# Optimization experiments

Measured on AMD Instinct MI355X. Metric: run time of the kernel, lower is better.

The kernel has to match this reference:

```python
import jax, jax.numpy as jnp
import numpy as np

N = 100_000      # num nodes
E = 1_600_000    # num edges
IN = 128         # in_channels
H = 256          # hidden_channels
BN_EPS = 1e-5
L2_EPS = 1e-12


def setup_inputs() -> dict:
    key = jax.random.key(0)
    ks = jax.random.split(key, 12)
    x = jax.random.normal(ks[0], (N, IN), dtype=jnp.float32)
    edge_index = jax.random.randint(ks[1], (2, E), 0, N, dtype=jnp.int64)
    edge_weight = jax.random.uniform(ks[2], (E,), dtype=jnp.float32)
    s_in = 1.0 / np.sqrt(IN)
    s_h = 1.0 / np.sqrt(H)
    return {
        "x": x,
        "edge_index": edge_index,
        "edge_weight": edge_weight,
        # lin0 (skip projection)
        "W0": jax.random.normal(ks[3], (H, IN), jnp.float32) * s_in,
        "b0": jnp.zeros((H,), jnp.float32),
        # conv1
        "W1": jax.random.normal(ks[4], (H, IN), jnp.float32) * s_in,
        "b1": jnp.zeros((H,), jnp.float32),
        "g1": jnp.ones((H,), jnp.float32),
        "be1": jnp.zeros((H,), jnp.float32),
        "m1": jax.random.normal(ks[5], (H,), jnp.float32) * 0.1,
        "v1": jax.random.uniform(ks[6], (H,), jnp.float32, 0.5, 1.5),
        # conv2
        "W2": jax.random.normal(ks[7], (H, H), jnp.float32) * s_h,
        "b2": jnp.zeros((H,), jnp.float32),
        "g2": jnp.ones((H,), jnp.float32),
        "be2": jnp.zeros((H,), jnp.float32),
        "m2": jax.random.normal(ks[8], (H,), jnp.float32) * 0.1,
        "v2": jax.random.uniform(ks[9], (H,), jnp.float32, 0.5, 1.5),
        # classifier
        "Wc": jax.random.normal(ks[10], (2, H), jnp.float32) * s_h,
        "bc": jnp.zeros((2,), jnp.float32),
    }


def _gcn_conv(x, src, dst, ew, W, b):
    """PyG GCNConv: D^-1/2 (A + I) D^-1/2 X W^T + b (self-loop weight 1)."""
    h = x @ W.T                                            # [N, out]
    deg = jax.ops.segment_sum(ew, dst, num_segments=N) + 1.0  # weighted in-degree incl. self-loop
    dinv = jnp.where(deg > 0, jax.lax.rsqrt(deg), 0.0)     # [N]
    norm = dinv[src] * ew * dinv[dst]                      # [E]
    agg = jax.ops.segment_sum(norm[:, None] * h[src], dst, num_segments=N)
    agg = agg + (dinv * dinv)[:, None] * h                 # self-loop term
    return agg + b


def _bn_eval(x, g, beta, m, v):
    return (x - m) * jax.lax.rsqrt(v + BN_EPS) * g + beta


def _l2norm(x):
    n = jnp.sqrt(jnp.sum(x * x, axis=1, keepdims=True))
    return x / jnp.maximum(n, L2_EPS)


def reference(x, edge_index, edge_weight, W0, b0, W1, b1, g1, be1, m1, v1,
              W2, b2, g2, be2, m2, v2, Wc, bc):
    src, dst = edge_index[0], edge_index[1]
    x0 = x @ W0.T + b0                                     # lin0 skip
    x1 = _gcn_conv(x, src, dst, edge_weight, W1, b1)
    x1 = jax.nn.relu(_bn_eval(x1, g1, be1, m1, v1))        # dropout = identity (eval)
    x1 = _l2norm(x1) + 0.2 * x0
    x2 = _gcn_conv(x1, src, dst, edge_weight, W2, b2)
    x2 = _bn_eval(x2, g2, be2, m2, v2)
    x2 = _l2norm(x2)
    embeddings = x2 + 0.5 * x1
    logits = embeddings @ Wc.T + bc
    return embeddings, logits
```

## Files before the change

kernel.cpp:

```cpp
#include <hip/hip_runtime.h>

#define NN 100000
#define EE 1600000
#define NBIN 391
#define CAPB 4864
#define TSCL 63.5f
#define TINV (1.0f / 63.5f)
#define XS   21.166666f
#define XSI  (6.0f / 127.0f)
#define WQS  16384.0f
#define WQI  (1.0f / 16384.0f)

typedef short bf16x8 __attribute__((ext_vector_type(8)));
typedef float f32x4 __attribute__((ext_vector_type(4)));

__device__ __forceinline__ float bl(unsigned int u) { return __uint_as_float(u << 16); }
__device__ __forceinline__ float bh(unsigned int u) { return __uint_as_float(u & 0xffff0000u); }
__device__ __forceinline__ unsigned short f2b(float f) {
  unsigned int u = __float_as_uint(f);
  return (unsigned short)((u + 0x7fffu + ((u >> 16) & 1u)) >> 16);
}
__device__ __forceinline__ float wsum(float v) {
#pragma unroll
  for (int o = 32; o; o >>= 1) v += __shfl_xor(v, o);
  return v;
}
__device__ __forceinline__ void g2l16(const void* g, void* l) {
  __builtin_amdgcn_global_load_lds((const __attribute__((address_space(1))) unsigned int*)g,
                                   (__attribute__((address_space(3))) unsigned int*)l, 16, 0, 0);
}
__device__ __forceinline__ int q8(float v, float lim, float sc) {
  return __float2int_rn(fminf(fmaxf(v, -lim), lim) * sc) & 0xff;
}
__device__ __forceinline__ int sx8(int u, int sh) { return (int)(signed char)(u >> sh); }

__global__ void k_zero(int* cnt, int n) {
  int i = blockIdx.x * 256 + threadIdx.x;
  if (i < n) cnt[i] = 0;
}

__global__ __launch_bounds__(256) void k_build(
    const int* __restrict__ src, const int* __restrict__ dst,
    const float* __restrict__ ew, int* gcnt, uint2* __restrict__ gbuf,
    const float* __restrict__ x, unsigned short* __restrict__ xb,
    unsigned int* __restrict__ xq8,
    const float* __restrict__ W1, const float* __restrict__ W0,
    const float* __restrict__ W2, unsigned short* __restrict__ Wcat,
    unsigned short* __restrict__ W2b)
{
  const int b = blockIdx.x;
  if (b < 391) {
    __shared__ uint2 est[4096];
    __shared__ int lhist[NBIN], lbase[NBIN], lcur[NBIN];
    const int tid = threadIdx.x;
    for (int t = tid; t < NBIN; t += 256) { lhist[t] = 0; lcur[t] = 0; }
    __syncthreads();
    const int e0 = b * 4096;
    const int ne = min(4096, EE - e0);
    for (int k = tid; k < ne; k += 256) {
      int e = e0 + k;
      int d = dst[e];
      int bin = d >> 8, low = d & 255;
      int q = min(__float2int_rn(ew[e] * 32768.0f), 32767);
      est[k] = make_uint2((unsigned)src[e],
                          ((unsigned)bin << 23) | ((unsigned)q << 8) | (unsigned)low);
      atomicAdd(&lhist[bin], 1);
    }
    __syncthreads();
    for (int t = tid; t < NBIN; t += 256)
      lbase[t] = lhist[t] ? atomicAdd(&gcnt[t], lhist[t]) : 0;
    __syncthreads();
    for (int k = tid; k < ne; k += 256) {
      uint2 E = est[k];
      int bin = E.y >> 23;
      int p = lbase[bin] + atomicAdd(&lcur[bin], 1);
      if (p < CAPB) gbuf[(size_t)bin * CAPB + p] = make_uint2(E.x, E.y & 0x7FFFFFu);
    }
  } else if (b < 12891) {
    int i = (b - 391) * 256 + threadIdx.x;
    float4 v = ((const float4*)x)[i];
    uint2 o;
    o.x = (unsigned int)f2b(v.x) | ((unsigned int)f2b(v.y) << 16);
    o.y = (unsigned int)f2b(v.z) | ((unsigned int)f2b(v.w) << 16);
    ((uint2*)xb)[i] = o;
    unsigned int p8 = (unsigned)q8(v.x, 6.f, XS) | ((unsigned)q8(v.y, 6.f, XS) << 8) |
                      ((unsigned)q8(v.z, 6.f, XS) << 16) | ((unsigned)q8(v.w, 6.f, XS) << 24);
    xq8[i] = p8;
  } else {
    int wb = b - 12891;
    const float* in;
    unsigned short* out;
    int idx;
    if (wb < 32)      { in = W1; out = Wcat;             idx = wb * 256 + threadIdx.x; }
    else if (wb < 64) { in = W0; out = Wcat + 256 * 128; idx = (wb - 32) * 256 + threadIdx.x; }
    else              { in = W2; out = W2b;              idx = (wb - 64) * 256 + threadIdx.x; }
    float4 v = ((const float4*)in)[idx];
    uint2 o;
    o.x = (unsigned int)f2b(v.x) | ((unsigned int)f2b(v.y) << 16);
    o.y = (unsigned int)f2b(v.z) | ((unsigned int)f2b(v.w) << 16);
    ((uint2*)out)[idx] = o;
  }
}

__global__ __launch_bounds__(256) void k_phase2(
    const uint2* __restrict__ gbuf, const int* __restrict__ gcnt,
    unsigned int* __restrict__ csr, int2* __restrict__ ntab, float* __restrict__ dinv)
{
  __shared__ uint2 ebuf[CAPB];
  __shared__ unsigned int obuf[CAPB];
  __shared__ int hist[256];
  __shared__ float wsm[256];
  __shared__ int cur[256];
  __shared__ int psum[256];
  const int g = blockIdx.x, tid = threadIdx.x;
  hist[tid] = 0; wsm[tid] = 0.f;
  __syncthreads();
  const int cn = min(gcnt[g], CAPB);
  for (int j = tid; j < cn; j += 256) {
    uint2 E = gbuf[(size_t)g * CAPB + j];
    ebuf[j] = E;
    int low = E.y & 255;
    atomicAdd(&hist[low], 1);
    atomicAdd(&wsm[low], (float)(E.y >> 8) * (1.0f / 32768.0f));
  }
  __syncthreads();
  int v = hist[tid];
  psum[tid] = v;
  __syncthreads();
  for (int off = 1; off < 256; off <<= 1) {
    int t = (tid >= off) ? psum[tid - off] : 0;
    __syncthreads();
    psum[tid] += t;
    __syncthreads();
  }
  int ex = psum[tid] - v;
  cur[tid] = ex;
  int node = g * 256 + tid;
  if (node < NN) {
    ntab[node] = make_int2(g * CAPB + ex, v);
    dinv[node] = rsqrtf(wsm[tid] + 1.0f);
  }
  __syncthreads();
  for (int j = tid; j < cn; j += 256) {
    uint2 E = ebuf[j];
    int low = E.y & 255;
    int p = atomicAdd(&cur[low], 1);
    obuf[p] = E.x | ((E.y >> 8) << 17);
  }
  __syncthreads();
  for (int j = tid; j < cn; j += 256) csr[(size_t)g * CAPB + j] = obuf[j];
}

__global__ __launch_bounds__(256) void k_aggregate8(
    const signed char* __restrict__ xq8, const int2* __restrict__ ntab,
    const unsigned int* __restrict__ csr, const float* __restrict__ dinv,
    unsigned short* __restrict__ ax)
{
  __shared__ int2 sm[4][64];
  const int wid = threadIdx.x >> 6, lane = threadIdx.x & 63;
  const int i = blockIdx.x * 4 + wid;
  const int2 nt = ntab[i];
  const int beg = nt.x, cn = nt.y;
  int acc0 = 0, acc1 = 0;
  for (int base = 0; base < cn; base += 64) {
    const int chunk = min(64, cn - base);
    int2 ent;
    if (lane < chunk) {
      unsigned int u = csr[beg + base + lane];
      int s = (int)(u & 0x1FFFFu);
      float nr = (float)(u >> 17) * (1.0f / 32768.0f) * dinv[s];
      ent = make_int2(s, __float2int_rn(nr * WQS));
    } else {
      ent = make_int2(i, 0);
    }
    sm[wid][lane] = ent;
    for (int sub = 0; sub < chunk; sub += 8) {
      int2 e[8];
#pragma unroll
      for (int k = 0; k < 8; ++k) e[k] = sm[wid][sub + k];
      int u[8];
#pragma unroll
      for (int k = 0; k < 8; ++k)
        u[k] = (int)*(const unsigned short*)(xq8 + (size_t)e[k].x * 128 + lane * 2);
#pragma unroll
      for (int k = 0; k < 8; ++k) {
        acc0 += __mul24(e[k].y, sx8(u[k], 0));
        acc1 += __mul24(e[k].y, sx8(u[k], 8));
      }
    }
  }
  const float di = dinv[i];
  const int di_q = __float2int_rn(di * WQS);
  int us = (int)*(const unsigned short*)(xq8 + (size_t)i * 128 + lane * 2);
  acc0 += __mul24(di_q, sx8(us, 0));
  acc1 += __mul24(di_q, sx8(us, 8));
  const float f = di * XSI * WQI;
  float r0 = f * (float)acc0;
  float r1 = f * (float)acc1;
  unsigned int o = (unsigned int)f2b(r0) | ((unsigned int)f2b(r1) << 16);
  *(unsigned int*)(ax + (size_t)i * 128 + lane * 2) = o;
}

__global__ __launch_bounds__(256) void k_mgemm(
    const unsigned short* __restrict__ A0, const unsigned short* __restrict__ A1, int nsplit,
    const unsigned short* __restrict__ B, unsigned short* __restrict__ C,
    int M, int K, int ldc)
{
  __shared__ __align__(16) unsigned short Als[128 * 64];
  __shared__ __align__(16) unsigned short Bls[128 * 64];
  const int tid = threadIdx.x;
  const int w = tid >> 6, l = tid & 63;
  const int m0 = blockIdx.x * 128, n0 = blockIdx.y * 128;
  const unsigned short* __restrict__ A = (n0 < nsplit) ? A0 : A1;
  const int wr = w >> 1, wc = w & 1;
  const int lr = l >> 3;
  const int lc = l & 7;
  const int fr = l & 15;
  const int fk = l >> 4;
  f32x4 acc[4][4];
#pragma unroll
  for (int m = 0; m < 4; ++m)
#pragma unroll
    for (int n = 0; n < 4; ++n)
#pragma unroll
      for (int q = 0; q < 4; ++q) acc[m][n][q] = 0.f;

  for (int k0 = 0; k0 < K; k0 += 64) {
#pragma unroll
    for (int i2 = 0; i2 < 4; ++i2) {
      const int ob = (w * 4 + i2) * 1024;
      const int r = (ob >> 7) + lr;
      const int c = lc ^ (r & 7);
      int rg = m0 + r; if (rg >= M) rg = M - 1;
      g2l16(A + (size_t)rg * K + k0 + c * 8, (char*)Als + ob);
      g2l16(B + (size_t)(n0 + r) * K + k0 + c * 8, (char*)Bls + ob);
    }
    __syncthreads();
#pragma unroll
    for (int ks = 0; ks < 2; ++ks) {
      bf16x8 af[4], bfr[4];
#pragma unroll
      for (int m = 0; m < 4; ++m) {
        const int r = wr * 64 + m * 16 + fr;
        const int cc = (ks * 4 + fk) ^ (r & 7);
        af[m] = *(const bf16x8*)((const char*)Als + r * 128 + cc * 16);
      }
#pragma unroll
      for (int n = 0; n < 4; ++n) {
        const int r = wc * 64 + n * 16 + fr;
        const int cc = (ks * 4 + fk) ^ (r & 7);
        bfr[n] = *(const bf16x8*)((const char*)Bls + r * 128 + cc * 16);
      }
#pragma unroll
      for (int m = 0; m < 4; ++m)
#pragma unroll
        for (int n = 0; n < 4; ++n)
          acc[m][n] = __builtin_amdgcn_mfma_f32_16x16x32_bf16(af[m], bfr[n], acc[m][n], 0, 0, 0);
    }
    __syncthreads();
  }
#pragma unroll
  for (int m = 0; m < 4; ++m) {
    const int rbase = m0 + wr * 64 + m * 16 + fk * 4;
#pragma unroll
    for (int n = 0; n < 4; ++n) {
      const int col = n0 + wc * 64 + n * 16 + fr;
#pragma unroll
      for (int q = 0; q < 4; ++q) {
        const int row = rbase + q;
        if (row < M) C[(size_t)row * ldc + col] = f2b(acc[m][n][q]);
      }
    }
  }
}

__global__ __launch_bounds__(256) void k_mgemmq(
    const unsigned short* __restrict__ A, const unsigned short* __restrict__ B,
    signed char* __restrict__ t8)
{
  __shared__ __align__(16) unsigned short Als[128 * 64];
  __shared__ __align__(16) unsigned short Bls[128 * 64];
  const int tid = threadIdx.x;
  const int w = tid >> 6, l = tid & 63;
  const int m0 = blockIdx.x * 128, n0 = blockIdx.y * 128;
  const int wr = w >> 1, wc = w & 1;
  const int lr = l >> 3;
  const int lc = l & 7;
  const int fr = l & 15;
  const int fk = l >> 4;
  f32x4 acc[4][4];
#pragma unroll
  for (int m = 0; m < 4; ++m)
#pragma unroll
    for (int n = 0; n < 4; ++n)
#pragma unroll
      for (int q = 0; q < 4; ++q) acc[m][n][q] = 0.f;

  for (int k0 = 0; k0 < 256; k0 += 64) {
#pragma unroll
    for (int i2 = 0; i2 < 4; ++i2) {
      const int ob = (w * 4 + i2) * 1024;
      const int r = (ob >> 7) + lr;
      const int c = lc ^ (r & 7);
      int rg = m0 + r; if (rg >= NN) rg = NN - 1;
      g2l16(A + (size_t)rg * 256 + k0 + c * 8, (char*)Als + ob);
      g2l16(B + (size_t)(n0 + r) * 256 + k0 + c * 8, (char*)Bls + ob);
    }
    __syncthreads();
#pragma unroll
    for (int ks = 0; ks < 2; ++ks) {
      bf16x8 af[4], bfr[4];
#pragma unroll
      for (int m = 0; m < 4; ++m) {
        const int r = wr * 64 + m * 16 + fr;
        const int cc = (ks * 4 + fk) ^ (r & 7);
        af[m] = *(const bf16x8*)((const char*)Als + r * 128 + cc * 16);
      }
#pragma unroll
      for (int n = 0; n < 4; ++n) {
        const int r = wc * 64 + n * 16 + fr;
        const int cc = (ks * 4 + fk) ^ (r & 7);
        bfr[n] = *(const bf16x8*)((const char*)Bls + r * 128 + cc * 16);
      }
#pragma unroll
      for (int m = 0; m < 4; ++m)
#pragma unroll
        for (int n = 0; n < 4; ++n)
          acc[m][n] = __builtin_amdgcn_mfma_f32_16x16x32_bf16(af[m], bfr[n], acc[m][n], 0, 0, 0);
    }
    __syncthreads();
  }
#pragma unroll
  for (int m = 0; m < 4; ++m) {
    const int rbase = m0 + wr * 64 + m * 16 + fk * 4;
#pragma unroll
    for (int n = 0; n < 4; ++n) {
      const int col = n0 + wc * 64 + n * 16 + fr;
#pragma unroll
      for (int q = 0; q < 4; ++q) {
        const int row = rbase + q;
        if (row < NN) {
          int qv = __float2int_rn(fminf(fmaxf(acc[m][n][q] * TSCL, -127.f), 127.f));
          t8[(size_t)row * 256 + col] = (signed char)qv;
        }
      }
    }
  }
}

__global__ __launch_bounds__(256) void k_post1(
    const unsigned short* __restrict__ C1, const float* __restrict__ b1,
    const float* __restrict__ g1, const float* __restrict__ be1,
    const float* __restrict__ m1, const float* __restrict__ v1,
    const float* __restrict__ b0, unsigned short* __restrict__ x1b)
{
  const int wid = threadIdx.x >> 6, lane = threadIdx.x & 63;
  const int i = blockIdx.x * 4 + wid;
  const int c0 = lane * 4;
  uint2 uh = *(const uint2*)(C1 + (size_t)i * 512 + c0);
  uint2 ux = *(const uint2*)(C1 + (size_t)i * 512 + 256 + c0);
  float hv[4] = {bl(uh.x), bh(uh.x), bl(uh.y), bh(uh.y)};
  float x0[4] = {bl(ux.x), bh(ux.x), bl(ux.y), bh(ux.y)};
  float ss = 0.f;
#pragma unroll
  for (int j = 0; j < 4; ++j) {
    const int c = c0 + j;
    float t = hv[j] + b1[c];
    t = (t - m1[c]) * rsqrtf(v1[c] + 1e-5f) * g1[c] + be1[c];
    t = fmaxf(t, 0.f);
    hv[j] = t;
    ss += t * t;
  }
  ss = wsum(ss);
  const float rn = 1.f / fmaxf(sqrtf(ss), 1e-12f);
  float r[4];
#pragma unroll
  for (int j = 0; j < 4; ++j) r[j] = fmaf(hv[j], rn, 0.2f * (x0[j] + b0[c0 + j]));
  uint2 o;
  o.x = (unsigned int)f2b(r[0]) | ((unsigned int)f2b(r[1]) << 16);
  o.y = (unsigned int)f2b(r[2]) | ((unsigned int)f2b(r[3]) << 16);
  *(uint2*)(x1b + (size_t)i * 256 + c0) = o;
}

__global__ __launch_bounds__(256) void k_aggpost2(
    const signed char* __restrict__ t8, const unsigned short* __restrict__ x1b,
    const int2* __restrict__ ntab, const unsigned int* __restrict__ csr,
    const float* __restrict__ dinv,
    const float* __restrict__ b2, const float* __restrict__ g2,
    const float* __restrict__ be2, const float* __restrict__ m2,
    const float* __restrict__ v2, const float* __restrict__ Wc,
    const float* __restrict__ bc, float* __restrict__ outE, float* __restrict__ outL)
{
  __shared__ int2 sm[4][64];
  const int wid = threadIdx.x >> 6, lane = threadIdx.x & 63;
  const int i = blockIdx.x * 4 + wid;
  const int c0 = lane * 4;
  const int2 nt = ntab[i];
  const int beg = nt.x, cn = nt.y;
  int acc[4] = {0, 0, 0, 0};
  for (int base = 0; base < cn; base += 64) {
    const int chunk = min(64, cn - base);
    int2 ent;
    if (lane < chunk) {
      unsigned int u = csr[beg + base + lane];
      int s = (int)(u & 0x1FFFFu);
      float nr = (float)(u >> 17) * (1.0f / 32768.0f) * dinv[s];
      ent = make_int2(s, __float2int_rn(nr * WQS));
    } else {
      ent = make_int2(i, 0);
    }
    sm[wid][lane] = ent;
    for (int sub = 0; sub < chunk; sub += 8) {
      int2 e[8];
#pragma unroll
      for (int k = 0; k < 8; ++k) e[k] = sm[wid][sub + k];
      int u[8];
#pragma unroll
      for (int k = 0; k < 8; ++k)
        u[k] = *(const int*)(t8 + (size_t)e[k].x * 256 + c0);
#pragma unroll
      for (int k = 0; k < 8; ++k) {
        acc[0] += __mul24(e[k].y, sx8(u[k], 0));
        acc[1] += __mul24(e[k].y, sx8(u[k], 8));
        acc[2] += __mul24(e[k].y, sx8(u[k], 16));
        acc[3] += __mul24(e[k].y, sx8(u[k], 24));
      }
    }
  }
  const float di = dinv[i];
  const int di_q = __float2int_rn(di * WQS);
  int usf = *(const int*)(t8 + (size_t)i * 256 + c0);
  acc[0] += __mul24(di_q, sx8(usf, 0));
  acc[1] += __mul24(di_q, sx8(usf, 8));
  acc[2] += __mul24(di_q, sx8(usf, 16));
  acc[3] += __mul24(di_q, sx8(usf, 24));
  uint2 uk = *(const uint2*)(x1b + (size_t)i * 256 + c0);
  float sk[4] = {bl(uk.x), bh(uk.x), bl(uk.y), bh(uk.y)};
  const float f = di * TINV * WQI;
  float ss = 0.f;
  float hv[4];
#pragma unroll
  for (int j = 0; j < 4; ++j) {
    const int c = c0 + j;
    float r = f * (float)acc[j] + b2[c];
    r = (r - m2[c]) * rsqrtf(v2[c] + 1e-5f) * g2[c] + be2[c];
    hv[j] = r;
    ss += r * r;
  }
  ss = wsum(ss);
  const float rn = 1.f / fmaxf(sqrtf(ss), 1e-12f);
  float e4[4];
  float s0 = 0.f, s1 = 0.f;
#pragma unroll
  for (int j = 0; j < 4; ++j) {
    e4[j] = fmaf(hv[j], rn, 0.5f * sk[j]);
    s0 = fmaf(e4[j], Wc[c0 + j], s0);
    s1 = fmaf(e4[j], Wc[256 + c0 + j], s1);
  }
  *(float4*)(outE + (size_t)i * 256 + c0) = make_float4(e4[0], e4[1], e4[2], e4[3]);
  s0 = wsum(s0);
  s1 = wsum(s1);
  if (lane == 0) {
    outL[(size_t)i * 2] = s0 + bc[0];
    outL[(size_t)i * 2 + 1] = s1 + bc[1];
  }
}

extern "C" void kernel_launch(void* const* d_in, const int* in_sizes, int n_in,
                              void* d_out, int out_size, void* d_ws, size_t ws_size,
                              hipStream_t stream) {
  const float* x   = (const float*)d_in[0];
  const int*   ei  = (const int*)d_in[1];
  const float* ew  = (const float*)d_in[2];
  const float* W0  = (const float*)d_in[3];
  const float* b0  = (const float*)d_in[4];
  const float* W1  = (const float*)d_in[5];
  const float* b1  = (const float*)d_in[6];
  const float* g1  = (const float*)d_in[7];
  const float* be1 = (const float*)d_in[8];
  const float* m1  = (const float*)d_in[9];
  const float* v1  = (const float*)d_in[10];
  const float* W2  = (const float*)d_in[11];
  const float* b2  = (const float*)d_in[12];
  const float* g2  = (const float*)d_in[13];
  const float* be2 = (const float*)d_in[14];
  const float* m2  = (const float*)d_in[15];
  const float* v2  = (const float*)d_in[16];
  const float* Wc  = (const float*)d_in[17];
  const float* bc  = (const float*)d_in[18];
  const int* srcp = ei;
  const int* dstp = ei + EE;

  char* w = (char*)d_ws;
  auto alloc = [&](size_t bytes) {
    char* p = w;
    w += (bytes + 255) & ~(size_t)255;
    return p;
  };
  unsigned short* xb     = (unsigned short*)alloc((size_t)NN * 128 * 2);
  unsigned int*   xq8    = (unsigned int*)alloc((size_t)NN * 128);
  unsigned short* ax     = (unsigned short*)alloc((size_t)NN * 128 * 2);
  unsigned short* x1b    = (unsigned short*)alloc((size_t)NN * 256 * 2);
  unsigned short* C1     = (unsigned short*)alloc((size_t)NN * 512 * 2);
  unsigned short* Wcat   = (unsigned short*)alloc((size_t)512 * 128 * 2);
  unsigned short* W2b    = (unsigned short*)alloc((size_t)256 * 256 * 2);
  signed char*    t8     = (signed char*)alloc((size_t)NN * 256);
  float*          dinvv  = (float*)alloc((size_t)NN * 4);
  int*            gcnt   = (int*)alloc((size_t)NBIN * 4);
  uint2*          gbuf   = (uint2*)alloc((size_t)NBIN * CAPB * 8);
  unsigned int*   csr    = (unsigned int*)alloc((size_t)NBIN * CAPB * 4);
  int2*           ntab   = (int2*)alloc((size_t)NN * 8);

  float* outEmb = (float*)d_out;
  float* outLog = outEmb + (size_t)NN * 256;

  const int NW = NN / 4;

  k_zero<<<2, 256, 0, stream>>>(gcnt, NBIN);
  k_build<<<13019, 256, 0, stream>>>(srcp, dstp, ew, gcnt, gbuf,
                                     x, xb, xq8, W1, W0, W2, Wcat, W2b);
  k_phase2<<<NBIN, 256, 0, stream>>>(gbuf, gcnt, csr, ntab, dinvv);

  k_aggregate8<<<NW, 256, 0, stream>>>((const signed char*)xq8, ntab, csr, dinvv, ax);
  dim3 g1d((NN + 127) / 128, 4);
  k_mgemm<<<g1d, 256, 0, stream>>>(ax, xb, 256, Wcat, C1, NN, 128, 512);
  k_post1<<<NW, 256, 0, stream>>>(C1, b1, g1, be1, m1, v1, b0, x1b);

  dim3 g2d((NN + 127) / 128, 2);
  k_mgemmq<<<g2d, 256, 0, stream>>>(x1b, W2b, t8);
  k_aggpost2<<<NW, 256, 0, stream>>>(t8, x1b, ntab, csr, dinvv,
                                     b2, g2, be2, m2, v2, Wc, bc, outEmb, outLog);
}
```

Baseline: 305.9 us.

## Fuse conv1 GEMM with BN/ReLU/L2-norm epilogue and split out skip GEMM

```diff
diff --git a/kernel.cpp b/kernel.cpp
--- a/kernel.cpp
+++ b/kernel.cpp
@@ -16,6 +16,7 @@
 
 __device__ __forceinline__ float bl(unsigned int u) { return __uint_as_float(u << 16); }
 __device__ __forceinline__ float bh(unsigned int u) { return __uint_as_float(u & 0xffff0000u); }
+__device__ __forceinline__ float b2f(unsigned short s) { return __uint_as_float((unsigned int)s << 16); }
 __device__ __forceinline__ unsigned short f2b(float f) {
   unsigned int u = __float_as_uint(f);
   return (unsigned short)((u + 0x7fffu + ((u >> 16) & 1u)) >> 16);
@@ -202,16 +203,14 @@
 }
 
 __global__ __launch_bounds__(256) void k_mgemm(
-    const unsigned short* __restrict__ A0, const unsigned short* __restrict__ A1, int nsplit,
-    const unsigned short* __restrict__ B, unsigned short* __restrict__ C,
-    int M, int K, int ldc)
+    const unsigned short* __restrict__ A, const unsigned short* __restrict__ B,
+    unsigned short* __restrict__ C, int M, int K, int ldc)
 {
   __shared__ __align__(16) unsigned short Als[128 * 64];
   __shared__ __align__(16) unsigned short Bls[128 * 64];
   const int tid = threadIdx.x;
   const int w = tid >> 6, l = tid & 63;
   const int m0 = blockIdx.x * 128, n0 = blockIdx.y * 128;
-  const unsigned short* __restrict__ A = (n0 < nsplit) ? A0 : A1;
   const int wr = w >> 1, wc = w & 1;
   const int lr = l >> 3;
   const int lc = l & 7;
@@ -272,6 +271,146 @@
       }
     }
   }
+}
+
+__global__ __launch_bounds__(256, 2) void k_gemm1f(
+    const unsigned short* __restrict__ A, const unsigned short* __restrict__ Wcat,
+    const unsigned short* __restrict__ x0b,
+    const float* __restrict__ b0, const float* __restrict__ b1,
+    const float* __restrict__ g1, const float* __restrict__ be1,
+    const float* __restrict__ m1, const float* __restrict__ v1,
+    unsigned short* __restrict__ x1b)
+{
+  __shared__ __align__(16) unsigned short Als[128 * 64];
+  __shared__ __align__(16) unsigned short Bls[256 * 64];
+  __shared__ float rss[2][128];
+  const int tid = threadIdx.x;
+  const int w = tid >> 6, l = tid & 63;
+  const int m0 = blockIdx.x * 128;
+  const int wr = w >> 1, wcb = w & 1;
+  const int lr = l >> 3, lc = l & 7, fr = l & 15, fk = l >> 4;
+  f32x4 acc[2][4][4];
+#pragma unroll
+  for (int ct = 0; ct < 2; ++ct)
+#pragma unroll
+    for (int m = 0; m < 4; ++m)
+#pragma unroll
+      for (int n = 0; n < 4; ++n)
+#pragma unroll
+        for (int qq = 0; qq < 4; ++qq) acc[ct][m][n][qq] = 0.f;
+
+  for (int k0 = 0; k0 < 128; k0 += 64) {
+#pragma unroll
+    for (int i2 = 0; i2 < 4; ++i2) {
+      const int ob = (w * 4 + i2) * 1024;
+      const int r = (ob >> 7) + lr;
+      const int c = lc ^ (r & 7);
+      int rg = m0 + r; if (rg >= NN) rg = NN - 1;
+      g2l16(A + (size_t)rg * 128 + k0 + c * 8, (char*)Als + ob);
+    }
+#pragma unroll
+    for (int i2 = 0; i2 < 8; ++i2) {
+      const int ob = (w * 8 + i2) * 1024;
+      const int r = (ob >> 7) + lr;
+      const int c = lc ^ (r & 7);
+      g2l16(Wcat + (size_t)r * 128 + k0 + c * 8, (char*)Bls + ob);
+    }
+    __syncthreads();
+#pragma unroll
+    for (int ks = 0; ks < 2; ++ks) {
+      bf16x8 af[4], bfr[2][4];
+#pragma unroll
+      for (int m = 0; m < 4; ++m) {
+        const int rA = wr * 64 + m * 16 + fr;
+        const int cc = (ks * 4 + fk) ^ (rA & 7);
+        af[m] = *(const bf16x8*)((const char*)Als + rA * 128 + cc * 16);
+      }
+#pragma unroll
+      for (int ct = 0; ct < 2; ++ct)
+#pragma unroll
+        for (int n = 0; n < 4; ++n) {
+          const int rB = (wcb + 2 * ct) * 64 + n * 16 + fr;
+          const int cc = (ks * 4 + fk) ^ (rB & 7);
+          bfr[ct][n] = *(const bf16x8*)((const char*)Bls + rB * 128 + cc * 16);
+        }
+#pragma unroll
+      for (int ct = 0; ct < 2; ++ct)
+#pragma unroll
+        for (int m = 0; m < 4; ++m)
+#pragma unroll
+          for (int n = 0; n < 4; ++n)
+            acc[ct][m][n] = __builtin_amdgcn_mfma_f32_16x16x32_bf16(af[m], bfr[ct][n], acc[ct][m][n], 0, 0, 0);
+    }
+    __syncthreads();
+  }
+
+  float A2[2][4], B2[2][4], C2[2][4];
+#pragma unroll
+  for (int ct = 0; ct < 2; ++ct)
+#pragma unroll
+    for (int n = 0; n < 4; ++n) {
+      const int c = (wcb + 2 * ct) * 64 + n * 16 + fr;
+      float sc = g1[c] * rsqrtf(v1[c] + 1e-5f);
+      A2[ct][n] = sc;
+      B2[ct][n] = (b1[c] - m1[c]) * sc + be1[c];
+      C2[ct][n] = 0.2f * b0[c];
+    }
+  float ssp[4][4];
+#pragma unroll
+  for (int m = 0; m < 4; ++m)
+#pragma unroll
+    for (int qq = 0; qq < 4; ++qq) ssp[m][qq] = 0.f;
+#pragma unroll
+  for (int ct = 0; ct < 2; ++ct)
+#pragma unroll
+    for (int m = 0; m < 4; ++m)
+#pragma unroll
+      for (int n = 0; n < 4; ++n)
+#pragma unroll
+        for (int qq = 0; qq < 4; ++qq) {
+          float t = fmaxf(acc[ct][m][n][qq] * A2[ct][n] + B2[ct][n], 0.f);
+          acc[ct][m][n][qq] = t;
+          ssp[m][qq] += t * t;
+        }
+#pragma unroll
+  for (int o = 1; o < 16; o <<= 1)
+#pragma unroll
+    for (int m = 0; m < 4; ++m)
+#pragma unroll
+      for (int qq = 0; qq < 4; ++qq) ssp[m][qq] += __shfl_xor(ssp[m][qq], o);
+  if (fr == 0) {
+#pragma unroll
+    for (int m = 0; m < 4; ++m)
+#pragma unroll
+      for (int qq = 0; qq < 4; ++qq)
+        rss[wcb][wr * 64 + m * 16 + fk * 4 + qq] = ssp[m][qq];
+  }
+  __syncthreads();
+  float rn[4][4];
+#pragma unroll
+  for (int m = 0; m < 4; ++m)
+#pragma unroll
+    for (int qq = 0; qq < 4; ++qq) {
+      const int r128 = wr * 64 + m * 16 + fk * 4 + qq;
+      rn[m][qq] = 1.f / fmaxf(sqrtf(rss[0][r128] + rss[1][r128]), 1e-12f);
+    }
+#pragma unroll
+  for (int ct = 0; ct < 2; ++ct)
+#pragma unroll
+    for (int m = 0; m < 4; ++m)
+#pragma unroll
+      for (int n = 0; n < 4; ++n) {
+        const int col = (wcb + 2 * ct) * 64 + n * 16 + fr;
+#pragma unroll
+        for (int qq = 0; qq < 4; ++qq) {
+          const int row = m0 + wr * 64 + m * 16 + fk * 4 + qq;
+          if (row < NN) {
+            float x0v = b2f(x0b[(size_t)row * 256 + col]);
+            float rv = acc[ct][m][n][qq] * rn[m][qq] + 0.2f * x0v + C2[ct][n];
+            x1b[(size_t)row * 256 + col] = f2b(rv);
+          }
+        }
+      }
 }
 
 __global__ __launch_bounds__(256) void k_mgemmq(
@@ -346,40 +485,6 @@
       }
     }
   }
-}
-
-__global__ __launch_bounds__(256) void k_post1(
-    const unsigned short* __restrict__ C1, const float* __restrict__ b1,
-    const float* __restrict__ g1, const float* __restrict__ be1,
-    const float* __restrict__ m1, const float* __restrict__ v1,
-    const float* __restrict__ b0, unsigned short* __restrict__ x1b)
-{
-  const int wid = threadIdx.x >> 6, lane = threadIdx.x & 63;
-  const int i = blockIdx.x * 4 + wid;
-  const int c0 = lane * 4;
-  uint2 uh = *(const uint2*)(C1 + (size_t)i * 512 + c0);
-  uint2 ux = *(const uint2*)(C1 + (size_t)i * 512 + 256 + c0);
-  float hv[4] = {bl(uh.x), bh(uh.x), bl(uh.y), bh(uh.y)};
-  float x0[4] = {bl(ux.x), bh(ux.x), bl(ux.y), bh(ux.y)};
-  float ss = 0.f;
-#pragma unroll
-  for (int j = 0; j < 4; ++j) {
-    const int c = c0 + j;
-    float t = hv[j] + b1[c];
-    t = (t - m1[c]) * rsqrtf(v1[c] + 1e-5f) * g1[c] + be1[c];
-    t = fmaxf(t, 0.f);
-    hv[j] = t;
-    ss += t * t;
-  }
-  ss = wsum(ss);
-  const float rn = 1.f / fmaxf(sqrtf(ss), 1e-12f);
-  float r[4];
-#pragma unroll
-  for (int j = 0; j < 4; ++j) r[j] = fmaf(hv[j], rn, 0.2f * (x0[j] + b0[c0 + j]));
-  uint2 o;
-  o.x = (unsigned int)f2b(r[0]) | ((unsigned int)f2b(r[1]) << 16);
-  o.y = (unsigned int)f2b(r[2]) | ((unsigned int)f2b(r[3]) << 16);
-  *(uint2*)(x1b + (size_t)i * 256 + c0) = o;
 }
 
 __global__ __launch_bounds__(256) void k_aggpost2(
@@ -500,8 +605,8 @@
   unsigned short* xb     = (unsigned short*)alloc((size_t)NN * 128 * 2);
   unsigned int*   xq8    = (unsigned int*)alloc((size_t)NN * 128);
   unsigned short* ax     = (unsigned short*)alloc((size_t)NN * 128 * 2);
+  unsigned short* x0b    = (unsigned short*)alloc((size_t)NN * 256 * 2);
   unsigned short* x1b    = (unsigned short*)alloc((size_t)NN * 256 * 2);
-  unsigned short* C1     = (unsigned short*)alloc((size_t)NN * 512 * 2);
   unsigned short* Wcat   = (unsigned short*)alloc((size_t)512 * 128 * 2);
   unsigned short* W2b    = (unsigned short*)alloc((size_t)256 * 256 * 2);
   signed char*    t8     = (signed char*)alloc((size_t)NN * 256);
@@ -521,10 +626,10 @@
                                      x, xb, xq8, W1, W0, W2, Wcat, W2b);
   k_phase2<<<NBIN, 256, 0, stream>>>(gbuf, gcnt, csr, ntab, dinvv);
 
+  dim3 g0d((NN + 127) / 128, 2);
+  k_mgemm<<<g0d, 256, 0, stream>>>(xb, Wcat + 256 * 128, x0b, NN, 128, 256);
   k_aggregate8<<<NW, 256, 0, stream>>>((const signed char*)xq8, ntab, csr, dinvv, ax);
-  dim3 g1d((NN + 127) / 128, 4);
-  k_mgemm<<<g1d, 256, 0, stream>>>(ax, xb, 256, Wcat, C1, NN, 128, 512);
-  k_post1<<<NW, 256, 0, stream>>>(C1, b1, g1, be1, m1, v1, b0, x1b);
+  k_gemm1f<<<782, 256, 0, stream>>>(ax, Wcat, x0b, b0, b1, g1, be1, m1, v1, x1b);
 
   dim3 g2d((NN + 127) / 128, 2);
   k_mgemmq<<<g2d, 256, 0, stream>>>(x1b, W2b, t8);
```

Measured after the change: 336.8 us. 1.1x slower.
